# Kernel tuning notes

Measured on AMD Instinct MI355X. Metric: run time of the kernel, lower is better.

The kernel has to match this reference:

```python
import jax, jax.numpy as jnp
import numpy as np

N, D, DB, E, H = 1024, 512, 64, 32768, 1024

def setup_inputs() -> dict:
    key = jax.random.key(0)
    k = jax.random.split(key, 6)
    object_feats = jax.random.normal(k[0], (N, D), dtype=jnp.float32)
    bboxes_embedding = jax.random.normal(k[1], (N, N, DB), dtype=jnp.float32)
    pairs = jax.random.randint(k[2], (E, 2), 0, N, dtype=jnp.int64)
    # Kaiming-normal-ish init for the two Linear layers
    W1 = jax.random.normal(k[3], (D + D + DB, H), dtype=jnp.float32) * np.sqrt(2.0 / (D + D + DB))
    b1 = jnp.zeros((H,), dtype=jnp.float32)
    W2 = jax.random.normal(k[4], (H, D), dtype=jnp.float32) * np.sqrt(2.0 / H)
    b2 = jnp.zeros((D,), dtype=jnp.float32)
    return {"object_feats": object_feats, "bboxes_embedding": bboxes_embedding,
            "pairs": pairs, "W1": W1, "b1": b1, "W2": W2, "b2": b2}

def reference(object_feats, bboxes_embedding, pairs, W1, b1, W2, b2):
    sub = pairs[:, 0]
    obj = pairs[:, 1]
    # gather pair features: [E, D] each, plus pairwise bbox embedding [E, DB]
    f_sub = object_feats[sub]
    f_obj = object_feats[obj]
    bb = bboxes_embedding[sub, obj]
    x = jnp.concatenate((f_sub, f_obj, bb), axis=1)  # [E, 2D+DB]
    h = jax.nn.relu(x @ W1 + b1)
    out = h @ W2 + b2  # [E, D]
    n = object_feats.shape[0]
    # scatter-mean into subject nodes; each node's own feature is included once,
    # so new_feat[i] = (object_feats[i] + sum_{pairs with sub==i} out) / (1 + count[i]).
    # Nodes with no incident pairs keep their original feature (count==0 -> identity).
    seg_sum = jax.ops.segment_sum(out, sub, num_segments=n)  # [N, D]
    count = jax.ops.segment_sum(jnp.ones((out.shape[0],), dtype=out.dtype), sub, num_segments=n)
    new_feats = (object_feats + seg_sum) / (1.0 + count)[:, None]
    return (new_feats, bboxes_embedding, pairs)
```

## Files before the change

### kernel.cpp

```cpp
#include <hip/hip_runtime.h>

#define N_OBJ 1024
#define E_P   32768

typedef float f32x4 __attribute__((ext_vector_type(4)));
typedef short bf16x8 __attribute__((ext_vector_type(8)));
typedef unsigned short u16x4 __attribute__((ext_vector_type(4)));

__device__ __forceinline__ unsigned short f2bf(float f) {
    unsigned u = __float_as_uint(f);
    u = u + 0x7FFFu + ((u >> 16) & 1u);
    return (unsigned short)(u >> 16);
}
__device__ __forceinline__ float bf2f(unsigned short u) {
    return __uint_as_float(((unsigned)u) << 16);
}

#define OFF_A    0
#define LEN_A    5242880
#define OFF_B    (OFF_A + LEN_A)
#define LEN_B    4194304
#define OFF_SEG  (OFF_B + LEN_B)
#define LEN_SEG  4194304
#define OFF_OUT  (OFF_SEG + LEN_SEG)
#define LEN_OUT  3145728

__device__ __forceinline__ void copy_nt(const f32x4* __restrict__ src,
                                        f32x4* __restrict__ dst,
                                        int off, int len, int nb, int cb) {
    int stride = nb * 256;
    int i = off + cb * 256 + threadIdx.x;
    int end = off + len;
    for (; i + 7 * stride < end; i += 8 * stride) {
        f32x4 v0 = __builtin_nontemporal_load(&src[i]);
        f32x4 v1 = __builtin_nontemporal_load(&src[i + stride]);
        f32x4 v2 = __builtin_nontemporal_load(&src[i + 2 * stride]);
        f32x4 v3 = __builtin_nontemporal_load(&src[i + 3 * stride]);
        f32x4 v4 = __builtin_nontemporal_load(&src[i + 4 * stride]);
        f32x4 v5 = __builtin_nontemporal_load(&src[i + 5 * stride]);
        f32x4 v6 = __builtin_nontemporal_load(&src[i + 6 * stride]);
        f32x4 v7 = __builtin_nontemporal_load(&src[i + 7 * stride]);
        __builtin_nontemporal_store(v0, &dst[i]);
        __builtin_nontemporal_store(v1, &dst[i + stride]);
        __builtin_nontemporal_store(v2, &dst[i + 2 * stride]);
        __builtin_nontemporal_store(v3, &dst[i + 3 * stride]);
        __builtin_nontemporal_store(v4, &dst[i + 4 * stride]);
        __builtin_nontemporal_store(v5, &dst[i + 5 * stride]);
        __builtin_nontemporal_store(v6, &dst[i + 6 * stride]);
        __builtin_nontemporal_store(v7, &dst[i + 7 * stride]);
    }
    for (; i < end; i += stride) {
        f32x4 a = __builtin_nontemporal_load(&src[i]);
        __builtin_nontemporal_store(a, &dst[i]);
    }
}

__global__ __launch_bounds__(256) void k_zero(int* __restrict__ counts) {
    ((int4*)counts)[threadIdx.x] = make_int4(0, 0, 0, 0);
}

__global__ __launch_bounds__(256) void k_a(const float* __restrict__ W1,
                                           const float* __restrict__ W2,
                                           const float* __restrict__ feats,
                                           const int* __restrict__ pairs,
                                           const float* __restrict__ bb,
                                           unsigned short* __restrict__ w1pqT,
                                           unsigned short* __restrict__ w1cT,
                                           unsigned short* __restrict__ w2T,
                                           unsigned short* __restrict__ featsb,
                                           float* __restrict__ out_pairs,
                                           int* __restrict__ counts,
                                           int* __restrict__ rank,
                                           unsigned short* __restrict__ bbgb,
                                           f32x4* __restrict__ hs4,
                                           const f32x4* __restrict__ csrc,
                                           f32x4* __restrict__ cdst) {
    int bid = blockIdx.x, tid = threadIdx.x;
    if ((bid % 3) == 2) { copy_nt(csrc, cdst, OFF_A, LEN_A, 1152, bid / 3); return; }
    int job = (bid / 3) * 2 + (bid % 3);
    if (job >= 2240) {
        int blk = job - 2240;
        f32x4 z = {0.f, 0.f, 0.f, 0.f};
        f32x4* p = hs4 + (size_t)blk * 4096 + tid;
        #pragma unroll
        for (int it = 0; it < 16; ++it) p[it * 256] = z;
        return;
    }
    if (job >= 2112) {
        int e = (job - 2112) * 256 + tid;
        int sub = pairs[2 * e], obj = pairs[2 * e + 1];
        const f32x4* src = (const f32x4*)&bb[((size_t)sub * 1024 + (size_t)obj) * 64];
        u16x4* dst = (u16x4*)&bbgb[(size_t)e * 64];
        #pragma unroll
        for (int i = 0; i < 16; ++i) {
            f32x4 v = __builtin_nontemporal_load(&src[i]);
            u16x4 o = { f2bf(v.x), f2bf(v.y), f2bf(v.z), f2bf(v.w) };
            dst[i] = o;
        }
        return;
    }
    if (job >= 1856) {
        int i = (job - 1856) * 256 + tid;
        out_pairs[i] = (float)pairs[i];
        if (i < E_P) rank[i] = atomicAdd(&counts[pairs[2 * i]], 1);
        return;
    }
    if (job >= 1600) {
        int base = (job - 1600) * 2048 + tid * 8;
        float4 v0 = *(const float4*)&feats[base];
        float4 v1 = *(const float4*)&feats[base + 4];
        u16x4 o0 = { f2bf(v0.x), f2bf(v0.y), f2bf(v0.z), f2bf(v0.w) };
        u16x4 o1 = { f2bf(v1.x), f2bf(v1.y), f2bf(v1.z), f2bf(v1.w) };
        *(u16x4*)&featsb[base] = o0;
        *(u16x4*)&featsb[base + 4] = o1;
        return;
    }
    const float* in; unsigned short* out;
    int LDI, LDO, r0, c0, nbase, kbase;
    if (job < 1024) {
        r0 = (job >> 5) * 32; c0 = (job & 31) * 32;
        in = W1; LDI = 1024; out = w1pqT; LDO = 512;
        nbase = c0 + (r0 >= 512 ? 1024 : 0); kbase = r0 & 511;
    } else if (job < 1088) {
        int t = job - 1024; r0 = 1024 + (t >> 5) * 32; c0 = (t & 31) * 32;
        in = W1; LDI = 1024; out = w1cT; LDO = 64;
        nbase = c0; kbase = r0 - 1024;
    } else {
        int t = job - 1088; r0 = (t >> 4) * 32; c0 = (t & 15) * 32;
        in = W2; LDI = 512; out = w2T; LDO = 1024;
        nbase = c0; kbase = r0;
    }
    __shared__ float lds[32][33];
    int ti = tid >> 3, tj = (tid & 7) * 4;
    float4 v = *(const float4*)&in[(size_t)(r0 + ti) * LDI + c0 + tj];
    lds[ti][tj] = v.x; lds[ti][tj + 1] = v.y; lds[ti][tj + 2] = v.z; lds[ti][tj + 3] = v.w;
    __syncthreads();
    int oc = tid >> 3, oj = (tid & 7) * 4;
    u16x4 o = { f2bf(lds[oj][oc]), f2bf(lds[oj + 1][oc]),
                f2bf(lds[oj + 2][oc]), f2bf(lds[oj + 3][oc]) };
    *(u16x4*)&out[(size_t)(nbase + oc) * LDO + kbase + oj] = o;
}

__global__ __launch_bounds__(256) void k_b(const int* __restrict__ counts,
                                           const int* __restrict__ rank,
                                           const int* __restrict__ pairs,
                                           int* __restrict__ csr_obj,
                                           int* __restrict__ csr_e,
                                           unsigned* __restrict__ brec,
                                           int* __restrict__ bcnt,
                                           const unsigned short* __restrict__ featsb,
                                           const unsigned short* __restrict__ w1pqT,
                                           const float* __restrict__ b1,
                                           float* __restrict__ P,
                                           unsigned short* __restrict__ Qb,
                                           const f32x4* __restrict__ csrc,
                                           f32x4* __restrict__ cdst) {
    int bid = blockIdx.x, tid = threadIdx.x;
    if ((bid % 3) < 2) { copy_nt(csrc, cdst, OFF_B, LEN_B, 1282, (bid / 3) * 2 + (bid % 3)); return; }
    int role = bid / 3;

    if (role >= 129) {
        int job = role - 129;
        int m0 = (job >> 5) * 64, n0 = (job & 31) * 64;
        int w = tid >> 6, l = tid & 63;
        int ln = l & 15, kb = (l >> 4) * 8;
        int row = m0 + w * 16 + ln;
        f32x4 acc[4] = {};
        for (int k0 = 0; k0 < 512; k0 += 32) {
            bf16x8 a = *(const bf16x8*)&featsb[(size_t)row * 512 + k0 + kb];
            #pragma unroll
            for (int f = 0; f < 4; ++f) {
                bf16x8 b = *(const bf16x8*)&w1pqT[(size_t)(n0 + f * 16 + ln) * 512 + k0 + kb];
                acc[f] = __builtin_amdgcn_mfma_f32_16x16x32_bf16(a, b, acc[f], 0, 0, 0);
            }
        }
        int mr = m0 + w * 16 + (l >> 4) * 4;
        if (n0 < 1024) {
            #pragma unroll
            for (int f = 0; f < 4; ++f) {
                int n = n0 + f * 16 + ln;
                float b1v = b1[n];
                #pragma unroll
                for (int r = 0; r < 4; ++r)
                    P[(size_t)(mr + r) * 1024 + n] = acc[f][r] + b1v;
            }
        } else {
            #pragma unroll
            for (int f = 0; f < 4; ++f) {
                int n = n0 - 1024 + f * 16 + ln;
                #pragma unroll
                for (int r = 0; r < 4; ++r)
                    Qb[(size_t)(mr + r) * 1024 + n] = f2bf(acc[f][r]);
            }
        }
        return;
    }

    __shared__ int sbuf[2][256];
    __shared__ int soff[1024];
    int c[4]; int s = 0;
    #pragma unroll
    for (int i = 0; i < 4; ++i) { c[i] = counts[tid * 4 + i]; s += c[i]; }
    sbuf[0][tid] = s;
    __syncthreads();
    int sel = 0;
    for (int d = 1; d < 256; d <<= 1) {
        int v = sbuf[sel][tid];
        if (tid >= d) v += sbuf[sel][tid - d];
        sbuf[sel ^ 1][tid] = v;
        sel ^= 1;
        __syncthreads();
    }
    int base = sbuf[sel][tid] - s;
    int run = base;
    #pragma unroll
    for (int i = 0; i < 4; ++i) { soff[tid * 4 + i] = run; run += c[i]; }
    __syncthreads();

    if (role >= 1) {
        int e = (role - 1) * 256 + tid;
        int sub = pairs[2 * e];
        int pos = soff[sub] + rank[e];
        csr_obj[pos] = pairs[2 * e + 1];
        csr_e[pos] = e;
        return;
    }

    int nb[4]; int t = 0;
    #pragma unroll
    for (int i = 0; i < 4; ++i) { nb[i] = (c[i] + 31) >> 5; t += nb[i]; }
    __syncthreads();
    sbuf[0][tid] = t;
    __syncthreads();
    sel = 0;
    for (int d = 1; d < 256; d <<= 1) {
        int v = sbuf[sel][tid];
        if (tid >= d) v += sbuf[sel][tid - d];
        sbuf[sel ^ 1][tid] = v;
        sel ^= 1;
        __syncthreads();
    }
    int bpos = sbuf[sel][tid] - t;
    int run2 = base;
    #pragma unroll
    for (int i = 0; i < 4; ++i) {
        int seg = tid * 4 + i;
        for (int k = 0; k < nb[i]; ++k) {
            int st = run2 + k * 32;
            int cnt = c[i] - k * 32; if (cnt > 32) cnt = 32;
            brec[bpos++] = (unsigned)st | ((unsigned)seg << 16) | ((unsigned)(cnt - 1) << 26);
        }
        run2 += c[i];
    }
    if (tid == 255) bcnt[0] = bpos;
}

__global__ __launch_bounds__(256) void k_seg(const int* __restrict__ csr_obj,
                                             const int* __restrict__ csr_e,
                                             const unsigned* __restrict__ brec,
                                             const int* __restrict__ bcnt,
                                             const unsigned short* __restrict__ bbgb,
                                             const unsigned short* __restrict__ w1cT,
                                             const float* __restrict__ P,
                                             const unsigned short* __restrict__ Qb,
                                             float* __restrict__ HS,
                                             const f32x4* __restrict__ csrc,
                                             f32x4* __restrict__ cdst) {
    int bid = blockIdx.x, tid = threadIdx.x;
    int x = bid & 7, k = bid >> 3;
    if (k >= 1024) { copy_nt(csrc, cdst, OFF_SEG, LEN_SEG, 4096, (k - 1024) * 8 + x); return; }
    int qd = x >> 1;
    int b = k * 2 + (x & 1);
    if (b >= bcnt[0]) return;
    unsigned rec = brec[b];
    const int start = rec & 0xFFFF;
    const int seg = (rec >> 16) & 0x3FF;
    const int n = ((rec >> 26) & 31) + 1;

    const int w = tid >> 6, l = tid & 63;
    const int ln = l & 15, g4 = l >> 4, kb = g4 * 8;
    const int cbase = qd * 256;
    const int wbase = cbase + w * 64;

    __shared__ unsigned short qs[32][264];

    {
        int p = tid >> 3, j = tid & 7;
        if (p < n) {
            int op = csr_obj[start + p];
            const uint4* qrow = (const uint4*)&Qb[(size_t)op * 1024 + cbase];
            #pragma unroll
            for (int i = 0; i < 4; ++i) {
                uint4 v = qrow[j * 4 + i];
                *(uint4*)&qs[p][(j * 4 + i) * 8] = v;
            }
        }
    }

    const int nA = n < 16 ? n : 16;
    const int nB = n - 16;
    int iA = start + (ln < nA ? ln : nA - 1);
    int iB = (nB > 0) ? (start + 16 + (ln < nB ? ln : nB - 1)) : iA;
    int eA = csr_e[iA];
    int eB = csr_e[iB];

    const unsigned short* brA = &bbgb[(size_t)eA * 64];
    const unsigned short* brB = &bbgb[(size_t)eB * 64];
    bf16x8 A0a = *(const bf16x8*)&brA[kb];
    bf16x8 A1a = *(const bf16x8*)&brA[32 + kb];
    bf16x8 A0b = *(const bf16x8*)&brB[kb];
    bf16x8 A1b = *(const bf16x8*)&brB[32 + kb];

    bool vA0 = (g4 * 4 + 0) < nA, vA1 = (g4 * 4 + 1) < nA;
    bool vA2 = (g4 * 4 + 2) < nA, vA3 = (g4 * 4 + 3) < nA;
    bool vB0 = (g4 * 4 + 0) < nB, vB1 = (g4 * 4 + 1) < nB;
    bool vB2 = (g4 * 4 + 2) < nB, vB3 = (g4 * 4 + 3) < nB;

    float pv[4];
    #pragma unroll
    for (int f = 0; f < 4; ++f)
        pv[f] = P[(size_t)seg * 1024 + wbase + f * 16 + ln];

    __syncthreads();

    #pragma unroll
    for (int f = 0; f < 4; ++f) {
        int col = wbase + f * 16 + ln;
        int cc = col - cbase;
        const unsigned short* wr = &w1cT[(size_t)col * 64];
        bf16x8 b0 = *(const bf16x8*)&wr[kb];
        bf16x8 b1 = *(const bf16x8*)&wr[32 + kb];
        f32x4 dA = {0.f, 0.f, 0.f, 0.f};
        dA = __builtin_amdgcn_mfma_f32_16x16x32_bf16(A0a, b0, dA, 0, 0, 0);
        dA = __builtin_amdgcn_mfma_f32_16x16x32_bf16(A1a, b1, dA, 0, 0, 0);
        f32x4 dB = {0.f, 0.f, 0.f, 0.f};
        dB = __builtin_amdgcn_mfma_f32_16x16x32_bf16(A0b, b0, dB, 0, 0, 0);
        dB = __builtin_amdgcn_mfma_f32_16x16x32_bf16(A1b, b1, dB, 0, 0, 0);
        float qA0 = bf2f(qs[g4 * 4 + 0][cc]);
        float qA1 = bf2f(qs[g4 * 4 + 1][cc]);
        float qA2 = bf2f(qs[g4 * 4 + 2][cc]);
        float qA3 = bf2f(qs[g4 * 4 + 3][cc]);
        float qB0 = bf2f(qs[16 + g4 * 4 + 0][cc]);
        float qB1 = bf2f(qs[16 + g4 * 4 + 1][cc]);
        float qB2 = bf2f(qs[16 + g4 * 4 + 2][cc]);
        float qB3 = bf2f(qs[16 + g4 * 4 + 3][cc]);
        float h = 0.f;
        h += vA0 ? fmaxf(dA[0] + pv[f] + qA0, 0.f) : 0.f;
        h += vA1 ? fmaxf(dA[1] + pv[f] + qA1, 0.f) : 0.f;
        h += vA2 ? fmaxf(dA[2] + pv[f] + qA2, 0.f) : 0.f;
        h += vA3 ? fmaxf(dA[3] + pv[f] + qA3, 0.f) : 0.f;
        h += vB0 ? fmaxf(dB[0] + pv[f] + qB0, 0.f) : 0.f;
        h += vB1 ? fmaxf(dB[1] + pv[f] + qB1, 0.f) : 0.f;
        h += vB2 ? fmaxf(dB[2] + pv[f] + qB2, 0.f) : 0.f;
        h += vB3 ? fmaxf(dB[3] + pv[f] + qB3, 0.f) : 0.f;
        h += __shfl_xor(h, 16);
        h += __shfl_xor(h, 32);
        if (l < 16) atomicAdd(&HS[(size_t)seg * 1024 + wbase + f * 16 + l], h);
    }
}

__global__ __launch_bounds__(256) void k_out(const float* __restrict__ HS,
                                             const unsigned short* __restrict__ w2T,
                                             const float* __restrict__ feats,
                                             const float* __restrict__ b2,
                                             const int* __restrict__ counts,
                                             float* __restrict__ out0,
                                             const f32x4* __restrict__ csrc,
                                             f32x4* __restrict__ cdst) {
    int bid = blockIdx.x;
    if ((bid % 17) != 16) { copy_nt(csrc, cdst, OFF_OUT, LEN_OUT, 2048, (bid / 17) * 16 + (bid % 17)); return; }
    int job = bid / 17;
    int m0 = (job >> 3) * 64, n0 = (job & 7) * 64;
    int tid = threadIdx.x, w = tid >> 6, l = tid & 63;
    int ln = l & 15, kb = (l >> 4) * 8;
    int row = m0 + w * 16 + ln;
    f32x4 acc[4] = {};
    for (int k0 = 0; k0 < 1024; k0 += 32) {
        const float* hp = &HS[(size_t)row * 1024 + k0 + kb];
        float4 h0 = *(const float4*)&hp[0];
        float4 h1 = *(const float4*)&hp[4];
        bf16x8 a;
        a[0] = (short)f2bf(h0.x); a[1] = (short)f2bf(h0.y); a[2] = (short)f2bf(h0.z); a[3] = (short)f2bf(h0.w);
        a[4] = (short)f2bf(h1.x); a[5] = (short)f2bf(h1.y); a[6] = (short)f2bf(h1.z); a[7] = (short)f2bf(h1.w);
        #pragma unroll
        for (int f = 0; f < 4; ++f) {
            bf16x8 b = *(const bf16x8*)&w2T[(size_t)(n0 + f * 16 + ln) * 1024 + k0 + kb];
            acc[f] = __builtin_amdgcn_mfma_f32_16x16x32_bf16(a, b, acc[f], 0, 0, 0);
        }
    }
    int mr = m0 + w * 16 + (l >> 4) * 4;
    float cv[4], inv[4];
    #pragma unroll
    for (int r = 0; r < 4; ++r) {
        float c = (float)counts[mr + r];
        cv[r] = c;
        inv[r] = 1.0f / (1.0f + c);
    }
    #pragma unroll
    for (int f = 0; f < 4; ++f) {
        int n = n0 + f * 16 + ln;
        float b2v = b2[n];
        #pragma unroll
        for (int r = 0; r < 4; ++r) {
            float fv = feats[(size_t)(mr + r) * 512 + n];
            out0[(size_t)(mr + r) * 512 + n] = (fv + acc[f][r] + cv[r] * b2v) * inv[r];
        }
    }
}

extern "C" void kernel_launch(void* const* d_in, const int* in_sizes, int n_in,
                              void* d_out, int out_size, void* d_ws, size_t ws_size,
                              hipStream_t stream) {
    const float* feats = (const float*)d_in[0];
    const float* bb    = (const float*)d_in[1];
    const int*   pairs = (const int*)d_in[2];
    const float* W1    = (const float*)d_in[3];
    const float* b1    = (const float*)d_in[4];
    const float* W2    = (const float*)d_in[5];
    const float* b2    = (const float*)d_in[6];

    float* out        = (float*)d_out;
    float* out_feats  = out;
    float* out_bb     = out + (size_t)N_OBJ * 512;
    float* out_pairs  = out + (size_t)N_OBJ * 512 + (size_t)N_OBJ * N_OBJ * 64;

    char* w = (char*)d_ws;
    unsigned short* featsb = (unsigned short*)w;
    unsigned short* w1pqT  = (unsigned short*)(w + (1u << 20));
    unsigned short* w1cT   = (unsigned short*)(w + (3u << 20));
    unsigned short* w2T    = (unsigned short*)(w + (3u << 20) + (128u << 10));
    float*          HS     = (float*)(w + (4u << 20) + (128u << 10));
    float*          P      = (float*)(w + (8u << 20) + (128u << 10));
    unsigned short* Qb     = (unsigned short*)(w + (12u << 20) + (128u << 10));
    unsigned short* bbgb   = (unsigned short*)(w + (14u << 20) + (128u << 10));
    char* ints = w + (18u << 20) + (128u << 10);
    int*      counts  = (int*)ints;
    int*      csr_obj = (int*)(ints + 4096);
    int*      csr_e   = (int*)(ints + 4096 + 131072);
    unsigned* brec    = (unsigned*)(ints + 4096 + 262144);
    int*      bcnt    = (int*)(ints + 4096 + 262144 + 16384);
    int*      rank    = (int*)(ints + 4096 + 262144 + 16384 + 64);

    const f32x4* cbb  = (const f32x4*)bb;
    f32x4*       cobb = (f32x4*)out_bb;

    k_zero<<<1, 256, 0, stream>>>(counts);

    k_a<<<3456, 256, 0, stream>>>(W1, W2, feats, pairs, bb, w1pqT, w1cT, w2T, featsb,
                                  out_pairs, counts, rank, bbgb, (f32x4*)HS, cbb, cobb);
    k_b<<<1923, 256, 0, stream>>>(counts, rank, pairs, csr_obj, csr_e, brec, bcnt,
                                  featsb, w1pqT, b1, P, Qb, cbb, cobb);
    k_seg<<<12288, 256, 0, stream>>>(csr_obj, csr_e, brec, bcnt, bbgb, w1cT, P, Qb, HS,
                                     cbb, cobb);
    k_out<<<2176, 256, 0, stream>>>(HS, w2T, feats, b2, counts, out_feats, cbb, cobb);
}
```

Measured before the change: 220.2 us.

## Process whole segments per block and gather bbox rows in CSR order

The segment kernel no longer splits each subject's edges into 32-edge records with atomic accumulation. Each block now loops over all edges of one subject segment and writes HS directly, which removes the HS zeroing pass, the brec/bcnt construction and the float atomics. The bbox gather moves into k_b, where rows are written in CSR order so k_seg reads them contiguously without the csr_e indirection. Launch sizes and the copy split are rebalanced to match, at the risk of load imbalance for segments with many edges.

```diff
diff --git a/kernel.cpp b/kernel.cpp
--- a/kernel.cpp
+++ b/kernel.cpp
@@ -31,23 +31,15 @@
     int stride = nb * 256;
     int i = off + cb * 256 + threadIdx.x;
     int end = off + len;
-    for (; i + 7 * stride < end; i += 8 * stride) {
+    for (; i + 3 * stride < end; i += 4 * stride) {
         f32x4 v0 = __builtin_nontemporal_load(&src[i]);
         f32x4 v1 = __builtin_nontemporal_load(&src[i + stride]);
         f32x4 v2 = __builtin_nontemporal_load(&src[i + 2 * stride]);
         f32x4 v3 = __builtin_nontemporal_load(&src[i + 3 * stride]);
-        f32x4 v4 = __builtin_nontemporal_load(&src[i + 4 * stride]);
-        f32x4 v5 = __builtin_nontemporal_load(&src[i + 5 * stride]);
-        f32x4 v6 = __builtin_nontemporal_load(&src[i + 6 * stride]);
-        f32x4 v7 = __builtin_nontemporal_load(&src[i + 7 * stride]);
         __builtin_nontemporal_store(v0, &dst[i]);
         __builtin_nontemporal_store(v1, &dst[i + stride]);
         __builtin_nontemporal_store(v2, &dst[i + 2 * stride]);
         __builtin_nontemporal_store(v3, &dst[i + 3 * stride]);
-        __builtin_nontemporal_store(v4, &dst[i + 4 * stride]);
-        __builtin_nontemporal_store(v5, &dst[i + 5 * stride]);
-        __builtin_nontemporal_store(v6, &dst[i + 6 * stride]);
-        __builtin_nontemporal_store(v7, &dst[i + 7 * stride]);
     }
     for (; i < end; i += stride) {
         f32x4 a = __builtin_nontemporal_load(&src[i]);
@@ -63,7 +55,6 @@
                                            const float* __restrict__ W2,
                                            const float* __restrict__ feats,
                                            const int* __restrict__ pairs,
-                                           const float* __restrict__ bb,
                                            unsigned short* __restrict__ w1pqT,
                                            unsigned short* __restrict__ w1cT,
                                            unsigned short* __restrict__ w2T,
@@ -71,34 +62,11 @@
                                            float* __restrict__ out_pairs,
                                            int* __restrict__ counts,
                                            int* __restrict__ rank,
-                                           unsigned short* __restrict__ bbgb,
-                                           f32x4* __restrict__ hs4,
                                            const f32x4* __restrict__ csrc,
                                            f32x4* __restrict__ cdst) {
     int bid = blockIdx.x, tid = threadIdx.x;
-    if ((bid % 3) == 2) { copy_nt(csrc, cdst, OFF_A, LEN_A, 1152, bid / 3); return; }
+    if ((bid % 3) == 2) { copy_nt(csrc, cdst, OFF_A, LEN_A, 1056, bid / 3); return; }
     int job = (bid / 3) * 2 + (bid % 3);
-    if (job >= 2240) {
-        int blk = job - 2240;
-        f32x4 z = {0.f, 0.f, 0.f, 0.f};
-        f32x4* p = hs4 + (size_t)blk * 4096 + tid;
-        #pragma unroll
-        for (int it = 0; it < 16; ++it) p[it * 256] = z;
-        return;
-    }
-    if (job >= 2112) {
-        int e = (job - 2112) * 256 + tid;
-        int sub = pairs[2 * e], obj = pairs[2 * e + 1];
-        const f32x4* src = (const f32x4*)&bb[((size_t)sub * 1024 + (size_t)obj) * 64];
-        u16x4* dst = (u16x4*)&bbgb[(size_t)e * 64];
-        #pragma unroll
-        for (int i = 0; i < 16; ++i) {
-            f32x4 v = __builtin_nontemporal_load(&src[i]);
-            u16x4 o = { f2bf(v.x), f2bf(v.y), f2bf(v.z), f2bf(v.w) };
-            dst[i] = o;
-        }
-        return;
-    }
     if (job >= 1856) {
         int i = (job - 1856) * 256 + tid;
         out_pairs[i] = (float)pairs[i];
@@ -144,10 +112,10 @@
 __global__ __launch_bounds__(256) void k_b(const int* __restrict__ counts,
                                            const int* __restrict__ rank,
                                            const int* __restrict__ pairs,
+                                           const float* __restrict__ bb,
                                            int* __restrict__ csr_obj,
-                                           int* __restrict__ csr_e,
-                                           unsigned* __restrict__ brec,
-                                           int* __restrict__ bcnt,
+                                           unsigned short* __restrict__ bbgc,
+                                           int* __restrict__ offsets,
                                            const unsigned short* __restrict__ featsb,
                                            const unsigned short* __restrict__ w1pqT,
                                            const float* __restrict__ b1,
@@ -217,49 +185,31 @@
     for (int i = 0; i < 4; ++i) { soff[tid * 4 + i] = run; run += c[i]; }
     __syncthreads();
 
-    if (role >= 1) {
-        int e = (role - 1) * 256 + tid;
-        int sub = pairs[2 * e];
-        int pos = soff[sub] + rank[e];
-        csr_obj[pos] = pairs[2 * e + 1];
-        csr_e[pos] = e;
+    if (role == 0) {
+        #pragma unroll
+        for (int i = 0; i < 4; ++i) offsets[tid * 4 + i] = soff[tid * 4 + i];
         return;
     }
 
-    int nb[4]; int t = 0;
-    #pragma unroll
-    for (int i = 0; i < 4; ++i) { nb[i] = (c[i] + 31) >> 5; t += nb[i]; }
-    __syncthreads();
-    sbuf[0][tid] = t;
-    __syncthreads();
-    sel = 0;
-    for (int d = 1; d < 256; d <<= 1) {
-        int v = sbuf[sel][tid];
-        if (tid >= d) v += sbuf[sel][tid - d];
-        sbuf[sel ^ 1][tid] = v;
-        sel ^= 1;
-        __syncthreads();
-    }
-    int bpos = sbuf[sel][tid] - t;
-    int run2 = base;
-    #pragma unroll
-    for (int i = 0; i < 4; ++i) {
-        int seg = tid * 4 + i;
-        for (int k = 0; k < nb[i]; ++k) {
-            int st = run2 + k * 32;
-            int cnt = c[i] - k * 32; if (cnt > 32) cnt = 32;
-            brec[bpos++] = (unsigned)st | ((unsigned)seg << 16) | ((unsigned)(cnt - 1) << 26);
-        }
-        run2 += c[i];
-    }
-    if (tid == 255) bcnt[0] = bpos;
+    int e = (role - 1) * 256 + tid;
+    int sub = pairs[2 * e];
+    int obj = pairs[2 * e + 1];
+    int pos = soff[sub] + rank[e];
+    csr_obj[pos] = obj;
+    const f32x4* src = (const f32x4*)&bb[((size_t)sub * 1024 + (size_t)obj) * 64];
+    u16x4* dst = (u16x4*)&bbgc[(size_t)pos * 64];
+    #pragma unroll
+    for (int i = 0; i < 16; ++i) {
+        f32x4 v = __builtin_nontemporal_load(&src[i]);
+        u16x4 o = { f2bf(v.x), f2bf(v.y), f2bf(v.z), f2bf(v.w) };
+        dst[i] = o;
+    }
 }
 
 __global__ __launch_bounds__(256) void k_seg(const int* __restrict__ csr_obj,
-                                             const int* __restrict__ csr_e,
-                                             const unsigned* __restrict__ brec,
-                                             const int* __restrict__ bcnt,
-                                             const unsigned short* __restrict__ bbgb,
+                                             const int* __restrict__ offsets,
+                                             const int* __restrict__ counts,
+                                             const unsigned short* __restrict__ bbgc,
                                              const unsigned short* __restrict__ w1cT,
                                              const float* __restrict__ P,
                                              const unsigned short* __restrict__ Qb,
@@ -268,14 +218,11 @@
                                              f32x4* __restrict__ cdst) {
     int bid = blockIdx.x, tid = threadIdx.x;
     int x = bid & 7, k = bid >> 3;
-    if (k >= 1024) { copy_nt(csrc, cdst, OFF_SEG, LEN_SEG, 4096, (k - 1024) * 8 + x); return; }
-    int qd = x >> 1;
-    int b = k * 2 + (x & 1);
-    if (b >= bcnt[0]) return;
-    unsigned rec = brec[b];
-    const int start = rec & 0xFFFF;
-    const int seg = (rec >> 16) & 0x3FF;
-    const int n = ((rec >> 26) & 31) + 1;
+    if (k >= 512) { copy_nt(csrc, cdst, OFF_SEG, LEN_SEG, 2048, (k - 512) * 8 + x); return; }
+    const int qd = x >> 1;
+    const int seg = k * 2 + (x & 1);
+    const int start = offsets[seg];
+    const int n = counts[seg];
 
     const int w = tid >> 6, l = tid & 63;
     const int ln = l & 15, g4 = l >> 4, kb = g4 * 8;
@@ -284,78 +231,88 @@
 
     __shared__ unsigned short qs[32][264];
 
-    {
-        int p = tid >> 3, j = tid & 7;
-        if (p < n) {
-            int op = csr_obj[start + p];
-            const uint4* qrow = (const uint4*)&Qb[(size_t)op * 1024 + cbase];
-            #pragma unroll
-            for (int i = 0; i < 4; ++i) {
-                uint4 v = qrow[j * 4 + i];
-                *(uint4*)&qs[p][(j * 4 + i) * 8] = v;
-            }
-        }
-    }
-
-    const int nA = n < 16 ? n : 16;
-    const int nB = n - 16;
-    int iA = start + (ln < nA ? ln : nA - 1);
-    int iB = (nB > 0) ? (start + 16 + (ln < nB ? ln : nB - 1)) : iA;
-    int eA = csr_e[iA];
-    int eB = csr_e[iB];
-
-    const unsigned short* brA = &bbgb[(size_t)eA * 64];
-    const unsigned short* brB = &bbgb[(size_t)eB * 64];
-    bf16x8 A0a = *(const bf16x8*)&brA[kb];
-    bf16x8 A1a = *(const bf16x8*)&brA[32 + kb];
-    bf16x8 A0b = *(const bf16x8*)&brB[kb];
-    bf16x8 A1b = *(const bf16x8*)&brB[32 + kb];
-
-    bool vA0 = (g4 * 4 + 0) < nA, vA1 = (g4 * 4 + 1) < nA;
-    bool vA2 = (g4 * 4 + 2) < nA, vA3 = (g4 * 4 + 3) < nA;
-    bool vB0 = (g4 * 4 + 0) < nB, vB1 = (g4 * 4 + 1) < nB;
-    bool vB2 = (g4 * 4 + 2) < nB, vB3 = (g4 * 4 + 3) < nB;
-
     float pv[4];
     #pragma unroll
     for (int f = 0; f < 4; ++f)
         pv[f] = P[(size_t)seg * 1024 + wbase + f * 16 + ln];
 
-    __syncthreads();
+    float hpart[4] = {0.f, 0.f, 0.f, 0.f};
+
+    for (int c0 = 0; c0 < n; c0 += 32) {
+        int m = n - c0; if (m > 32) m = 32;
+        const int mA = m < 16 ? m : 16;
+        const int mB = m - 16;
+
+        __syncthreads();
+        {
+            int p = tid >> 3, j = tid & 7;
+            if (p < m) {
+                int op = csr_obj[start + c0 + p];
+                const uint4* qrow = (const uint4*)&Qb[(size_t)op * 1024 + cbase];
+                #pragma unroll
+                for (int i = 0; i < 4; ++i) {
+                    uint4 v = qrow[j * 4 + i];
+                    *(uint4*)&qs[p][(j * 4 + i) * 8] = v;
+                }
+            }
+        }
+
+        int iA = start + c0 + (ln < mA ? ln : mA - 1);
+        int iB = (mB > 0) ? (start + c0 + 16 + (ln < mB ? ln : mB - 1)) : iA;
+        const unsigned short* brA = &bbgc[(size_t)iA * 64];
+        const unsigned short* brB = &bbgc[(size_t)iB * 64];
+        bf16x8 A0a = *(const bf16x8*)&brA[kb];
+        bf16x8 A1a = *(const bf16x8*)&brA[32 + kb];
+        bf16x8 A0b = *(const bf16x8*)&brB[kb];
+        bf16x8 A1b = *(const bf16x8*)&brB[32 + kb];
+
+        bool vA0 = (g4 * 4 + 0) < mA, vA1 = (g4 * 4 + 1) < mA;
+        bool vA2 = (g4 * 4 + 2) < mA, vA3 = (g4 * 4 + 3) < mA;
+        bool vB0 = (g4 * 4 + 0) < mB, vB1 = (g4 * 4 + 1) < mB;
+        bool vB2 = (g4 * 4 + 2) < mB, vB3 = (g4 * 4 + 3) < mB;
+
+        __syncthreads();
+
+        #pragma unroll
+        for (int f = 0; f < 4; ++f) {
+            int col = wbase + f * 16 + ln;
+            int cc = col - cbase;
+            const unsigned short* wr = &w1cT[(size_t)col * 64];
+            bf16x8 b0 = *(const bf16x8*)&wr[kb];
+            bf16x8 b1 = *(const bf16x8*)&wr[32 + kb];
+            f32x4 dA = {0.f, 0.f, 0.f, 0.f};
+            dA = __builtin_amdgcn_mfma_f32_16x16x32_bf16(A0a, b0, dA, 0, 0, 0);
+            dA = __builtin_amdgcn_mfma_f32_16x16x32_bf16(A1a, b1, dA, 0, 0, 0);
+            f32x4 dB = {0.f, 0.f, 0.f, 0.f};
+            dB = __builtin_amdgcn_mfma_f32_16x16x32_bf16(A0b, b0, dB, 0, 0, 0);
+            dB = __builtin_amdgcn_mfma_f32_16x16x32_bf16(A1b, b1, dB, 0, 0, 0);
+            float qA0 = bf2f(qs[g4 * 4 + 0][cc]);
+            float qA1 = bf2f(qs[g4 * 4 + 1][cc]);
+            float qA2 = bf2f(qs[g4 * 4 + 2][cc]);
+            float qA3 = bf2f(qs[g4 * 4 + 3][cc]);
+            float qB0 = bf2f(qs[16 + g4 * 4 + 0][cc]);
+            float qB1 = bf2f(qs[16 + g4 * 4 + 1][cc]);
+            float qB2 = bf2f(qs[16 + g4 * 4 + 2][cc]);
+            float qB3 = bf2f(qs[16 + g4 * 4 + 3][cc]);
+            float h = 0.f;
+            h += vA0 ? fmaxf(dA[0] + pv[f] + qA0, 0.f) : 0.f;
+            h += vA1 ? fmaxf(dA[1] + pv[f] + qA1, 0.f) : 0.f;
+            h += vA2 ? fmaxf(dA[2] + pv[f] + qA2, 0.f) : 0.f;
+            h += vA3 ? fmaxf(dA[3] + pv[f] + qA3, 0.f) : 0.f;
+            h += vB0 ? fmaxf(dB[0] + pv[f] + qB0, 0.f) : 0.f;
+            h += vB1 ? fmaxf(dB[1] + pv[f] + qB1, 0.f) : 0.f;
+            h += vB2 ? fmaxf(dB[2] + pv[f] + qB2, 0.f) : 0.f;
+            h += vB3 ? fmaxf(dB[3] + pv[f] + qB3, 0.f) : 0.f;
+            hpart[f] += h;
+        }
+    }
 
     #pragma unroll
     for (int f = 0; f < 4; ++f) {
-        int col = wbase + f * 16 + ln;
-        int cc = col - cbase;
-        const unsigned short* wr = &w1cT[(size_t)col * 64];
-        bf16x8 b0 = *(const bf16x8*)&wr[kb];
-        bf16x8 b1 = *(const bf16x8*)&wr[32 + kb];
-        f32x4 dA = {0.f, 0.f, 0.f, 0.f};
-        dA = __builtin_amdgcn_mfma_f32_16x16x32_bf16(A0a, b0, dA, 0, 0, 0);
-        dA = __builtin_amdgcn_mfma_f32_16x16x32_bf16(A1a, b1, dA, 0, 0, 0);
-        f32x4 dB = {0.f, 0.f, 0.f, 0.f};
-        dB = __builtin_amdgcn_mfma_f32_16x16x32_bf16(A0b, b0, dB, 0, 0, 0);
-        dB = __builtin_amdgcn_mfma_f32_16x16x32_bf16(A1b, b1, dB, 0, 0, 0);
-        float qA0 = bf2f(qs[g4 * 4 + 0][cc]);
-        float qA1 = bf2f(qs[g4 * 4 + 1][cc]);
-        float qA2 = bf2f(qs[g4 * 4 + 2][cc]);
-        float qA3 = bf2f(qs[g4 * 4 + 3][cc]);
-        float qB0 = bf2f(qs[16 + g4 * 4 + 0][cc]);
-        float qB1 = bf2f(qs[16 + g4 * 4 + 1][cc]);
-        float qB2 = bf2f(qs[16 + g4 * 4 + 2][cc]);
-        float qB3 = bf2f(qs[16 + g4 * 4 + 3][cc]);
-        float h = 0.f;
-        h += vA0 ? fmaxf(dA[0] + pv[f] + qA0, 0.f) : 0.f;
-        h += vA1 ? fmaxf(dA[1] + pv[f] + qA1, 0.f) : 0.f;
-        h += vA2 ? fmaxf(dA[2] + pv[f] + qA2, 0.f) : 0.f;
-        h += vA3 ? fmaxf(dA[3] + pv[f] + qA3, 0.f) : 0.f;
-        h += vB0 ? fmaxf(dB[0] + pv[f] + qB0, 0.f) : 0.f;
-        h += vB1 ? fmaxf(dB[1] + pv[f] + qB1, 0.f) : 0.f;
-        h += vB2 ? fmaxf(dB[2] + pv[f] + qB2, 0.f) : 0.f;
-        h += vB3 ? fmaxf(dB[3] + pv[f] + qB3, 0.f) : 0.f;
+        float h = hpart[f];
         h += __shfl_xor(h, 16);
         h += __shfl_xor(h, 32);
-        if (l < 16) atomicAdd(&HS[(size_t)seg * 1024 + wbase + f * 16 + l], h);
+        if (l < 16) HS[(size_t)seg * 1024 + wbase + f * 16 + l] = h;
     }
 }
 
@@ -432,25 +389,23 @@
     float*          HS     = (float*)(w + (4u << 20) + (128u << 10));
     float*          P      = (float*)(w + (8u << 20) + (128u << 10));
     unsigned short* Qb     = (unsigned short*)(w + (12u << 20) + (128u << 10));
-    unsigned short* bbgb   = (unsigned short*)(w + (14u << 20) + (128u << 10));
+    unsigned short* bbgc   = (unsigned short*)(w + (14u << 20) + (128u << 10));
     char* ints = w + (18u << 20) + (128u << 10);
     int*      counts  = (int*)ints;
-    int*      csr_obj = (int*)(ints + 4096);
-    int*      csr_e   = (int*)(ints + 4096 + 131072);
-    unsigned* brec    = (unsigned*)(ints + 4096 + 262144);
-    int*      bcnt    = (int*)(ints + 4096 + 262144 + 16384);
-    int*      rank    = (int*)(ints + 4096 + 262144 + 16384 + 64);
+    int*      offsets = (int*)(ints + 4096);
+    int*      csr_obj = (int*)(ints + 8192);
+    int*      rank    = (int*)(ints + 8192 + 131072);
 
     const f32x4* cbb  = (const f32x4*)bb;
     f32x4*       cobb = (f32x4*)out_bb;
 
     k_zero<<<1, 256, 0, stream>>>(counts);
 
-    k_a<<<3456, 256, 0, stream>>>(W1, W2, feats, pairs, bb, w1pqT, w1cT, w2T, featsb,
-                                  out_pairs, counts, rank, bbgb, (f32x4*)HS, cbb, cobb);
-    k_b<<<1923, 256, 0, stream>>>(counts, rank, pairs, csr_obj, csr_e, brec, bcnt,
+    k_a<<<3168, 256, 0, stream>>>(W1, W2, feats, pairs, w1pqT, w1cT, w2T, featsb,
+                                  out_pairs, counts, rank, cbb, cobb);
+    k_b<<<1923, 256, 0, stream>>>(counts, rank, pairs, bb, csr_obj, bbgc, offsets,
                                   featsb, w1pqT, b1, P, Qb, cbb, cobb);
-    k_seg<<<12288, 256, 0, stream>>>(csr_obj, csr_e, brec, bcnt, bbgb, w1cT, P, Qb, HS,
-                                     cbb, cobb);
+    k_seg<<<6144, 256, 0, stream>>>(csr_obj, offsets, counts, bbgc, w1cT, P, Qb, HS,
+                                    cbb, cobb);
     k_out<<<2176, 256, 0, stream>>>(HS, w2T, feats, b2, counts, out_feats, cbb, cobb);
 }
```

Result: faster. 215.8 us (-2.0%).
